# Optimization experiments

Hardware: AMD Instinct MI355X
Metric: run time of the kernel (lower is better)

The kernel has to match this reference:

```python
import jax, jax.numpy as jnp
import numpy as np

NUM_NODES = 100000
NFEAT = 128
EMBED_DIM = 128
NHEADS = 2
NHID = EMBED_DIM // NHEADS  # 64
REL_DIM = 128
NUM_REL = 500
E1 = 288000  # 1-hop edges
E2 = 32000   # 2-hop edges
E = E1 + E2
ALPHA = 0.2  # LeakyReLU slope
EPS = 1e-16


def setup_inputs() -> dict:
    key = jax.random.key(0)
    ks = jax.random.split(key, 10)
    edge_index = jax.random.randint(ks[0], (2, E), 0, NUM_NODES, dtype=jnp.int32)
    x = jax.random.normal(ks[1], (NUM_NODES, NFEAT), dtype=jnp.float32)
    r = jax.random.normal(ks[2], (NUM_REL, REL_DIM), dtype=jnp.float32)
    edge_type = jax.random.randint(ks[3], (E1,), 0, NUM_REL, dtype=jnp.int32)
    edge_type_nhop = jax.random.randint(ks[4], (E2, 2), 0, NUM_REL, dtype=jnp.int32)
    # learned params (get_param -> xavier-ish normal)
    s = 0.02
    W_heads = jax.random.normal(ks[5], (NHEADS, 2 * NFEAT + REL_DIM, NHID), dtype=jnp.float32) * s
    a_heads = jax.random.normal(ks[6], (NHEADS, NHID, 1), dtype=jnp.float32) * s
    W_out = jax.random.normal(ks[7], (2 * (NHID * NHEADS) + EMBED_DIM, NHEADS * NHID), dtype=jnp.float32) * s
    a_out = jax.random.normal(ks[8], (NHEADS * NHID, 1), dtype=jnp.float32) * s
    W_r = jax.random.normal(ks[9], (REL_DIM, EMBED_DIM), dtype=jnp.float32) * s
    return {"edge_index": edge_index, "x": x, "r": r, "edge_type": edge_type,
            "edge_type_nhop": edge_type_nhop, "W_heads": W_heads, "a_heads": a_heads,
            "W_out": W_out, "a_out": a_out, "W_r": W_r}


def _gat_layer(edge_index, x, edge_embed, W, a, concat):
    src = edge_index[0]
    dst = edge_index[1]
    # [E, 2*in + rel] -> [E, out]
    edge_h = jnp.concatenate([x[src], x[dst], edge_embed], axis=1) @ W
    e = jax.nn.leaky_relu(jnp.squeeze(edge_h @ a, axis=-1), negative_slope=ALPHA)  # [E]
    # segment softmax over src groups
    seg_max = jax.ops.segment_max(e, src, num_segments=NUM_NODES)
    w = jnp.exp(e - seg_max[src])
    denom = jax.ops.segment_sum(w, src, num_segments=NUM_NODES)
    att = w / (denom[src] + EPS)  # dropout p=0.0 -> identity
    out = jax.ops.segment_sum(att[:, None] * edge_h, src, num_segments=NUM_NODES)  # [N, out]
    return jax.nn.elu(out) if concat else out


def reference(edge_index, x, r, edge_type, edge_type_nhop, W_heads, a_heads, W_out, a_out, W_r):
    # first-pass relation edge embeddings
    edge_embed = jnp.concatenate(
        [r[edge_type], r[edge_type_nhop[:, 0]] + r[edge_type_nhop[:, 1]]], axis=0)  # [E, rel]
    # multi-head attention layers (concat heads)
    heads = [_gat_layer(edge_index, x, edge_embed, W_heads[h], a_heads[h], True)
             for h in range(NHEADS)]
    x1 = jnp.concatenate(heads, axis=1)  # [N, nheads*nhid]; dropout p=0 identity
    # transform relations
    r2 = r @ W_r  # [num_rel, embed_dim]
    edge_embed2 = jnp.concatenate(
        [r2[edge_type], r2[edge_type_nhop[:, 0]] + r2[edge_type_nhop[:, 1]]], axis=0)
    out = jax.nn.elu(_gat_layer(edge_index, x1, edge_embed2, W_out, a_out, False))
    return out, r2
```

## Files before the change

### kernel.cpp

```cpp
#include <hip/hip_runtime.h>
#include <math.h>

#define NNODES 100000
#define NREL 500
#define E1 288000
#define ETOT 320000
#define LALPHA 0.2f
#define SEPS 1e-16f
#define NB_SCAN ((NNODES + 255) / 256)
#define GTILES 6250
#define GTPB 5
#define GGRID (GTILES / GTPB)

typedef __attribute__((ext_vector_type(8))) short bf16x8;
typedef __attribute__((ext_vector_type(4))) float f32x4;

__device__ __forceinline__ unsigned short f2bf(float x) {
  unsigned int u = __float_as_uint(x);
  unsigned int r = (u + 0x7fffu + ((u >> 16) & 1u)) >> 16;
  return (unsigned short)r;
}
__device__ __forceinline__ unsigned int packbf2(float lo, float hi) {
  return (unsigned int)f2bf(lo) | ((unsigned int)f2bf(hi) << 16);
}
__device__ __forceinline__ float unpk_lo(unsigned int u) { return __uint_as_float(u << 16); }
__device__ __forceinline__ float unpk_hi(unsigned int u) {
  return __uint_as_float(u & 0xffff0000u);
}
__device__ __forceinline__ float lrelu(float e) { return (e >= 0.f) ? e : LALPHA * e; }
__device__ __forceinline__ float wexp(float lg) { return __expf(fminf(lg, 60.f)); }

__device__ __forceinline__ float wave_sum64(float v) {
#pragma unroll
  for (int o = 32; o >= 1; o >>= 1) v += __shfl_xor(v, o, 64);
  return v;
}
__device__ __forceinline__ float red16(float v) {
  v += __shfl_xor(v, 1, 64);
  v += __shfl_xor(v, 2, 64);
  v += __shfl_xor(v, 4, 64);
  v += __shfl_xor(v, 8, 64);
  return v;
}

__global__ void k_zero_int(int* __restrict__ p, int n) {
  int i = blockIdx.x * blockDim.x + threadIdx.x;
  if (i < n) p[i] = 0;
}

__global__ void k_count(const int* __restrict__ src, int* __restrict__ cnt) {
  int e = blockIdx.x * blockDim.x + threadIdx.x;
  if (e < ETOT) atomicAdd(&cnt[src[e]], 1);
}

__global__ void k_scan_a(const int* __restrict__ cnt, int* __restrict__ rowstart,
                         int* __restrict__ blockTot) {
  __shared__ int s[256];
  int t = threadIdx.x;
  int idx = blockIdx.x * 256 + t;
  int v = (idx < NNODES) ? cnt[idx] : 0;
  s[t] = v;
  __syncthreads();
  for (int off = 1; off < 256; off <<= 1) {
    int xv = (t >= off) ? s[t - off] : 0;
    __syncthreads();
    s[t] += xv;
    __syncthreads();
  }
  if (idx < NNODES) rowstart[idx] = s[t] - v;
  if (t == 255) blockTot[blockIdx.x] = s[255];
}

__global__ void k_scan_b(const int* __restrict__ blockTot, int* __restrict__ blockOff) {
  __shared__ int s[512];
  int t = threadIdx.x;
  int v = (t < NB_SCAN) ? blockTot[t] : 0;
  s[t] = v;
  __syncthreads();
  for (int off = 1; off < 512; off <<= 1) {
    int xv = (t >= off) ? s[t - off] : 0;
    __syncthreads();
    s[t] += xv;
    __syncthreads();
  }
  if (t < NB_SCAN) blockOff[t] = s[t] - v;
}

__global__ void k_scan_c(int* __restrict__ rowstart, const int* __restrict__ blockOff,
                         int* __restrict__ cursor) {
  int idx = blockIdx.x * 256 + threadIdx.x;
  if (idx < NNODES) {
    int v = rowstart[idx] + blockOff[blockIdx.x];
    rowstart[idx] = v;
    cursor[idx] = v;
  }
  if (idx == 0) rowstart[NNODES] = ETOT;
}

__global__ void k_scatter(const int* __restrict__ srcA, const int* __restrict__ dstA,
                          const int* __restrict__ et, const int* __restrict__ et2,
                          int* __restrict__ cursor, int* __restrict__ dnp,
                          int2* __restrict__ t12) {
  int e = blockIdx.x * blockDim.x + threadIdx.x;
  if (e < ETOT) {
    int pos = atomicAdd(&cursor[srcA[e]], 1);
    dnp[pos] = dstA[e];
    int t1, t2 = -1;
    if (e < E1) {
      t1 = et[e];
    } else {
      int2 tt = ((const int2*)et2)[e - E1];
      t1 = tt.x;
      t2 = tt.y;
    }
    t12[pos] = make_int2(t1, t2);
  }
}

__global__ void k_relprep1(const float* __restrict__ r, const float* __restrict__ Wh,
                           const float* __restrict__ ah, unsigned int* __restrict__ rW1p,
                           float* __restrict__ srel1) {
  __shared__ float vals[128];
  int t = blockIdx.x;
  int tid = threadIdx.x;
  int h = tid >> 6, kk = tid & 63;
  const float* wcol = Wh + h * 24576 + 256 * 64 + kk;
  const float* rrow = r + t * 128;
  float acc = 0.f;
#pragma unroll 4
  for (int d = 0; d < 128; ++d) acc = fmaf(rrow[d], wcol[d * 64], acc);
  vals[tid] = acc;
  float p = wave_sum64(acc * ah[h * 64 + kk]);
  if (kk == 0) srel1[t * 2 + h] = p;
  __syncthreads();
  if (tid < 64) rW1p[t * 64 + tid] = packbf2(vals[2 * tid], vals[2 * tid + 1]);
}

__global__ void k_relprep2f(const float* __restrict__ r, const float* __restrict__ Wr,
                            const float* __restrict__ Wo, const float* __restrict__ ao,
                            unsigned int* __restrict__ rW2p, float* __restrict__ srel2,
                            float* __restrict__ r2out) {
  __shared__ float v2[128];
  __shared__ float s[128];
  __shared__ float vals[128];
  int t = blockIdx.x;
  int k = threadIdx.x;
  float a2 = 0.f;
#pragma unroll 4
  for (int d = 0; d < 128; ++d) a2 = fmaf(r[t * 128 + d], Wr[d * 128 + k], a2);
  r2out[t * 128 + k] = a2;
  v2[k] = a2;
  __syncthreads();
  float acc = 0.f;
#pragma unroll 4
  for (int d = 0; d < 128; ++d) acc = fmaf(v2[d], Wo[(256 + d) * 128 + k], acc);
  vals[k] = acc;
  s[k] = acc * ao[k];
  __syncthreads();
  for (int off = 64; off >= 1; off >>= 1) {
    if (k < off) s[k] += s[k + off];
    __syncthreads();
  }
  if (k == 0) srel2[t] = s[0];
  if (k < 64) rW2p[t * 64 + k] = packbf2(vals[2 * k], vals[2 * k + 1]);
}

__global__ void k_packb_both(const float* __restrict__ Wh, const float* __restrict__ Wo,
                             unsigned short* __restrict__ Wb1,
                             unsigned short* __restrict__ Wb2) {
  int c = blockIdx.x & 255;
  int layer = blockIdx.x >> 8;
  int d = threadIdx.x;
  if (layer == 0) {
    int h = (c >> 6) & 1, part = c >> 7, kc = c & 63;
    Wb1[c * 128 + d] = f2bf(Wh[h * 24576 + (part * 128 + d) * 64 + kc]);
  } else {
    int part = c >> 7, kc = c & 127;
    Wb2[c * 128 + d] = f2bf(Wo[(part * 128 + d) * 128 + kc]);
  }
}

template <int LAYER>
__global__ __launch_bounds__(256) void k_gemm_mfma(const void* __restrict__ Xin,
                                                   const unsigned short* __restrict__ Wb,
                                                   const float* __restrict__ avec,
                                                   unsigned int* __restrict__ xWp,
                                                   float* __restrict__ sc) {
  const int lane = threadIdx.x & 63;
  const int wave = threadIdx.x >> 6;
  const int colv = lane & 15;
  const int kg = lane >> 4;

  bf16x8 b[4][4];
#pragma unroll
  for (int t = 0; t < 4; ++t)
#pragma unroll
    for (int s = 0; s < 4; ++s)
      b[t][s] = *(const bf16x8*)(Wb + (size_t)(wave * 64 + t * 16 + colv) * 128 + s * 32 +
                                 kg * 8);
  float av[4];
#pragma unroll
  for (int t = 0; t < 4; ++t) av[t] = avec[(wave & 1) * 64 + t * 16 + colv];
  const int slot = (LAYER == 1) ? (((wave & 1) << 1) | (wave >> 1)) : wave;

  const float4* xf4 = (const float4*)Xin;
  const uint4* xu4 = (const uint4*)Xin;
  int tile = blockIdx.x * GTPB;

  float4 cf[8];
  uint4 cu[4];
  {
    int ar = tile * 16 + colv;
    if (LAYER == 1) {
      int base = ar * 32 + kg * 2;
#pragma unroll
      for (int s = 0; s < 4; ++s) {
        cf[2 * s] = xf4[base + s * 8];
        cf[2 * s + 1] = xf4[base + s * 8 + 1];
      }
    } else {
      int base = ar * 16 + kg;
#pragma unroll
      for (int s = 0; s < 4; ++s) cu[s] = xu4[base + s * 4];
    }
  }

  for (int it = 0; it < GTPB; ++it, ++tile) {
    float4 nf[8];
    uint4 nu[4];
    const bool hasnext = (it + 1 < GTPB);
    if (hasnext) {
      int ar = (tile + 1) * 16 + colv;
      if (LAYER == 1) {
        int base = ar * 32 + kg * 2;
#pragma unroll
        for (int s = 0; s < 4; ++s) {
          nf[2 * s] = xf4[base + s * 8];
          nf[2 * s + 1] = xf4[base + s * 8 + 1];
        }
      } else {
        int base = ar * 16 + kg;
#pragma unroll
        for (int s = 0; s < 4; ++s) nu[s] = xu4[base + s * 4];
      }
    }

    bf16x8 a[4];
    if (LAYER == 1) {
#pragma unroll
      for (int s = 0; s < 4; ++s) {
        union {
          unsigned short us[8];
          bf16x8 v;
        } u;
        u.us[0] = f2bf(cf[2 * s].x); u.us[1] = f2bf(cf[2 * s].y);
        u.us[2] = f2bf(cf[2 * s].z); u.us[3] = f2bf(cf[2 * s].w);
        u.us[4] = f2bf(cf[2 * s + 1].x); u.us[5] = f2bf(cf[2 * s + 1].y);
        u.us[6] = f2bf(cf[2 * s + 1].z); u.us[7] = f2bf(cf[2 * s + 1].w);
        a[s] = u.v;
      }
    } else {
#pragma unroll
      for (int s = 0; s < 4; ++s) {
        union {
          uint4 q;
          bf16x8 v;
        } u;
        u.q = cu[s];
        a[s] = u.v;
      }
    }

    f32x4 acc[4];
#pragma unroll
    for (int t = 0; t < 4; ++t) acc[t] = (f32x4){0.f, 0.f, 0.f, 0.f};
#pragma unroll
    for (int s = 0; s < 4; ++s)
#pragma unroll
      for (int t = 0; t < 4; ++t)
        acc[t] = __builtin_amdgcn_mfma_f32_16x16x32_bf16(a[s], b[t][s], acc[t], 0, 0, 0);

    const int rbase = tile * 16 + kg * 4;
    const int m = colv >> 1;
    const bool evn = (colv & 1) == 0;
#pragma unroll
    for (int i = 0; i < 4; ++i) {
      unsigned int* orow = xWp + (size_t)(rbase + i) * 128 + wave * 32;
#pragma unroll
      for (int t = 0; t < 4; ++t) {
        float lo = acc[t][i];
        float other = __shfl_xor(lo, 1, 64);
        if (evn) orow[t * 8 + m] = packbf2(lo, other);
      }
      float p = 0.f;
#pragma unroll
      for (int t = 0; t < 4; ++t) p = fmaf(acc[t][i], av[t], p);
      p = red16(p);
      if (colv == 0) sc[(size_t)(rbase + i) * 4 + slot] = p;
    }

    if (hasnext) {
      if (LAYER == 1) {
#pragma unroll
        for (int j = 0; j < 8; ++j) cf[j] = nf[j];
      } else {
#pragma unroll
        for (int j = 0; j < 4; ++j) cu[j] = nu[j];
      }
    }
  }
}

__global__ __launch_bounds__(256) void k_agg1(
    const int* __restrict__ rowstart, const int* __restrict__ dnp,
    const int2* __restrict__ t12, const unsigned int* __restrict__ xWp,
    const unsigned int* __restrict__ rW1p, const float* __restrict__ sc1,
    const float2* __restrict__ srel1, unsigned int* __restrict__ x1b) {
  int n = blockIdx.x * 4 + (threadIdx.x >> 6);
  int lane = threadIdx.x & 63;
  int q = lane & 15, g = lane >> 4;
  int s0 = rowstart[n];
  int deg = rowstart[n + 1] - s0;
  int jj = q + 16 * g;
  float r0 = 0.f, r1 = 0.f;
  if (deg > 0) {
    float4 scn = ((const float4*)sc1)[n];
    const float ss0 = scn.x, ss1 = scn.z;
    float ac0[4] = {0.f, 0.f, 0.f, 0.f}, ac1[4] = {0.f, 0.f, 0.f, 0.f};
    float dsum0 = 0.f, dsum1 = 0.f;
    const int pend = s0 + deg;
    for (int p0 = s0; p0 < pend; p0 += 4) {
      int p = p0 + g;
      float w0 = 0.f, w1 = 0.f;
      int dne = 0, t1e = 0, t2e = -1;
      if (p < pend) {
        dne = dnp[p];
        int2 tt = t12[p];
        t1e = tt.x;
        t2e = tt.y;
        float2 sr = srel1[t1e];
        float rel0 = sr.x, rel1 = sr.y;
        if (t2e >= 0) {
          float2 sb = srel1[t2e];
          rel0 += sb.x;
          rel1 += sb.y;
        }
        float4 sdv = ((const float4*)sc1)[dne];
        w0 = wexp(lrelu(ss0 + sdv.y + rel0));
        w1 = wexp(lrelu(ss1 + sdv.w + rel1));
        dsum0 += w0;
        dsum1 += w1;
      }
      const unsigned int* xr = xWp + (size_t)dne * 128 + 64;
      const unsigned int* rp = rW1p + (size_t)t1e * 64;
#pragma unroll
      for (int k = 0; k < 4; ++k) {
        int j2 = q + 16 * k;
        float as = (k < 2) ? w0 : w1;
        unsigned int ud = xr[j2];
        unsigned int ur = rp[j2];
        float rv0 = unpk_lo(ur), rv1 = unpk_hi(ur);
        if (t2e >= 0) {
          unsigned int u2 = rW1p[(size_t)t2e * 64 + j2];
          rv0 += unpk_lo(u2);
          rv1 += unpk_hi(u2);
        }
        ac0[k] = fmaf(as, unpk_lo(ud) + rv0, ac0[k]);
        ac1[k] = fmaf(as, unpk_hi(ud) + rv1, ac1[k]);
      }
    }
#pragma unroll
    for (int k = 0; k < 4; ++k) {
      ac0[k] += __shfl_xor(ac0[k], 16, 64);
      ac0[k] += __shfl_xor(ac0[k], 32, 64);
      ac1[k] += __shfl_xor(ac1[k], 16, 64);
      ac1[k] += __shfl_xor(ac1[k], 32, 64);
    }
    dsum0 += __shfl_xor(dsum0, 16, 64);
    dsum0 += __shfl_xor(dsum0, 32, 64);
    dsum1 += __shfl_xor(dsum1, 16, 64);
    dsum1 += __shfl_xor(dsum1, 32, 64);
    float a0g = (g == 0) ? ac0[0] : (g == 1) ? ac0[1] : (g == 2) ? ac0[2] : ac0[3];
    float a1g = (g == 0) ? ac1[0] : (g == 1) ? ac1[1] : (g == 2) ? ac1[2] : ac1[3];
    float dsel = (g < 2) ? dsum0 : dsum1;
    float isel = 1.f / (dsel + SEPS);
    unsigned int us = xWp[(size_t)n * 128 + jj];
    float o0 = (a0g + dsel * unpk_lo(us)) * isel;
    float o1 = (a1g + dsel * unpk_hi(us)) * isel;
    r0 = (o0 > 0.f) ? o0 : __expf(o0) - 1.f;
    r1 = (o1 > 0.f) ? o1 : __expf(o1) - 1.f;
  }
  x1b[(size_t)n * 64 + jj] = packbf2(r0, r1);
}

__global__ __launch_bounds__(256) void k_agg2(
    const int* __restrict__ rowstart, const int* __restrict__ dnp,
    const int2* __restrict__ t12, const unsigned int* __restrict__ xWp,
    const unsigned int* __restrict__ rW2p, const float* __restrict__ sc2,
    const float* __restrict__ srel2, float* __restrict__ outp) {
  int n = blockIdx.x * 4 + (threadIdx.x >> 6);
  int lane = threadIdx.x & 63;
  int q = lane & 15, g = lane >> 4;
  int s0 = rowstart[n];
  int deg = rowstart[n + 1] - s0;
  int jj = q + 16 * g;
  float r0 = 0.f, r1 = 0.f;
  if (deg > 0) {
    float4 scn = ((const float4*)sc2)[n];
    const float ss = scn.x + scn.y;
    float ac0[4] = {0.f, 0.f, 0.f, 0.f}, ac1[4] = {0.f, 0.f, 0.f, 0.f};
    float dsum = 0.f;
    const int pend = s0 + deg;
    for (int p0 = s0; p0 < pend; p0 += 4) {
      int p = p0 + g;
      float w = 0.f;
      int dne = 0, t1e = 0, t2e = -1;
      if (p < pend) {
        dne = dnp[p];
        int2 tt = t12[p];
        t1e = tt.x;
        t2e = tt.y;
        float rel = srel2[t1e];
        if (t2e >= 0) rel += srel2[t2e];
        float4 sdv = ((const float4*)sc2)[dne];
        w = wexp(lrelu(ss + (sdv.z + sdv.w) + rel));
        dsum += w;
      }
      const unsigned int* xr = xWp + (size_t)dne * 128 + 64;
      const unsigned int* rp = rW2p + (size_t)t1e * 64;
#pragma unroll
      for (int k = 0; k < 4; ++k) {
        int j2 = q + 16 * k;
        unsigned int ud = xr[j2];
        unsigned int ur = rp[j2];
        float rv0 = unpk_lo(ur), rv1 = unpk_hi(ur);
        if (t2e >= 0) {
          unsigned int u2 = rW2p[(size_t)t2e * 64 + j2];
          rv0 += unpk_lo(u2);
          rv1 += unpk_hi(u2);
        }
        ac0[k] = fmaf(w, unpk_lo(ud) + rv0, ac0[k]);
        ac1[k] = fmaf(w, unpk_hi(ud) + rv1, ac1[k]);
      }
    }
#pragma unroll
    for (int k = 0; k < 4; ++k) {
      ac0[k] += __shfl_xor(ac0[k], 16, 64);
      ac0[k] += __shfl_xor(ac0[k], 32, 64);
      ac1[k] += __shfl_xor(ac1[k], 16, 64);
      ac1[k] += __shfl_xor(ac1[k], 32, 64);
    }
    dsum += __shfl_xor(dsum, 16, 64);
    dsum += __shfl_xor(dsum, 32, 64);
    float a0g = (g == 0) ? ac0[0] : (g == 1) ? ac0[1] : (g == 2) ? ac0[2] : ac0[3];
    float a1g = (g == 0) ? ac1[0] : (g == 1) ? ac1[1] : (g == 2) ? ac1[2] : ac1[3];
    float inv = 1.f / (dsum + SEPS);
    unsigned int us = xWp[(size_t)n * 128 + jj];
    float o0 = (a0g + dsum * unpk_lo(us)) * inv;
    float o1 = (a1g + dsum * unpk_hi(us)) * inv;
    r0 = (o0 > 0.f) ? o0 : __expf(o0) - 1.f;
    r1 = (o1 > 0.f) ? o1 : __expf(o1) - 1.f;
  }
  ((float2*)outp)[(size_t)n * 64 + jj] = make_float2(r0, r1);
}

extern "C" void kernel_launch(void* const* d_in, const int* in_sizes, int n_in, void* d_out,
                              int out_size, void* d_ws, size_t ws_size, hipStream_t stream) {
  const int* edge_index = (const int*)d_in[0];
  const int* srcA = edge_index;
  const int* dstA = edge_index + ETOT;
  const float* x = (const float*)d_in[1];
  const float* r = (const float*)d_in[2];
  const int* et = (const int*)d_in[3];
  const int* et2 = (const int*)d_in[4];
  const float* Wh = (const float*)d_in[5];
  const float* ah = (const float*)d_in[6];
  const float* Wo = (const float*)d_in[7];
  const float* ao = (const float*)d_in[8];
  const float* Wr = (const float*)d_in[9];
  float* out = (float*)d_out;
  float* r2out = out + (size_t)NNODES * 128;

  char* ws = (char*)d_ws;
  size_t o = 0;
  auto alloc = [&](size_t bytes) {
    char* p = ws + o;
    o += (bytes + 255) & ~(size_t)255;
    return p;
  };
  unsigned int* xWp = (unsigned int*)alloc((size_t)NNODES * 128 * 4);
  float* sc1 = (float*)alloc((size_t)NNODES * 4 * 4);
  float* sc2 = (float*)alloc((size_t)NNODES * 4 * 4);
  unsigned int* rW1p = (unsigned int*)alloc((size_t)NREL * 64 * 4);
  float* srel1 = (float*)alloc(2 * NREL * 4);
  unsigned int* rW2p = (unsigned int*)alloc((size_t)NREL * 64 * 4);
  float* srel2 = (float*)alloc(NREL * 4);
  unsigned int* x1b = (unsigned int*)alloc((size_t)NNODES * 64 * 4);
  unsigned short* Wb1 = (unsigned short*)alloc(256 * 128 * 2);
  unsigned short* Wb2 = (unsigned short*)alloc(256 * 128 * 2);
  int* cnt = (int*)alloc(NNODES * 4);
  int* rowstart = (int*)alloc((NNODES + 1) * 4);
  int* cursor = (int*)alloc(NNODES * 4);
  int* blockTot = (int*)alloc(512 * 4);
  int* blockOff = (int*)alloc(512 * 4);
  int* dnp = (int*)alloc(ETOT * 4);
  int2* t12 = (int2*)alloc((size_t)ETOT * 8);

  const int EB = (ETOT + 255) / 256;

  k_zero_int<<<(NNODES + 255) / 256, 256, 0, stream>>>(cnt, NNODES);
  k_count<<<EB, 256, 0, stream>>>(srcA, cnt);
  k_scan_a<<<NB_SCAN, 256, 0, stream>>>(cnt, rowstart, blockTot);
  k_scan_b<<<1, 512, 0, stream>>>(blockTot, blockOff);
  k_scan_c<<<NB_SCAN, 256, 0, stream>>>(rowstart, blockOff, cursor);
  k_scatter<<<EB, 256, 0, stream>>>(srcA, dstA, et, et2, cursor, dnp, t12);

  k_relprep1<<<NREL, 128, 0, stream>>>(r, Wh, ah, rW1p, srel1);
  k_relprep2f<<<NREL, 128, 0, stream>>>(r, Wr, Wo, ao, rW2p, srel2, r2out);
  k_packb_both<<<512, 128, 0, stream>>>(Wh, Wo, Wb1, Wb2);

  k_gemm_mfma<1><<<GGRID, 256, 0, stream>>>(x, Wb1, ah, xWp, sc1);
  k_agg1<<<NNODES / 4, 256, 0, stream>>>(rowstart, dnp, t12, xWp, rW1p, sc1,
                                         (const float2*)srel1, x1b);

  k_gemm_mfma<2><<<GGRID, 256, 0, stream>>>(x1b, Wb2, ao, xWp, sc2);
  k_agg2<<<NNODES / 4, 256, 0, stream>>>(rowstart, dnp, t12, xWp, rW2p, sc2, srel2, out);
}
```

Measured before the change: 392.7 us.

## Merge prep kernels and fuse scatter with layer-1 GEMM; vectorize aggregation gathers

Folds the edge counting, both relation-projection kernels and the weight packing into one launch, and runs the CSR scatter and the layer-1 MFMA GEMM as separate block ranges of a single kernel. This cuts the number of launches and lets independent work overlap. The aggregation kernels now use 16-byte uint4 gathers per lane with a remapped output column order (jo = 4q+g) instead of four scalar 4-byte loads. That remap has to match the packed GEMM layout, so it carries a risk of permuting columns.

```diff
diff --git a/kernel.cpp b/kernel.cpp
--- a/kernel.cpp
+++ b/kernel.cpp
@@ -11,6 +11,7 @@
 #define GTILES 6250
 #define GTPB 5
 #define GGRID (GTILES / GTPB)
+#define EB 1250
 
 typedef __attribute__((ext_vector_type(8))) short bf16x8;
 typedef __attribute__((ext_vector_type(4))) float f32x4;
@@ -46,11 +47,6 @@
 __global__ void k_zero_int(int* __restrict__ p, int n) {
   int i = blockIdx.x * blockDim.x + threadIdx.x;
   if (i < n) p[i] = 0;
-}
-
-__global__ void k_count(const int* __restrict__ src, int* __restrict__ cnt) {
-  int e = blockIdx.x * blockDim.x + threadIdx.x;
-  if (e < ETOT) atomicAdd(&cnt[src[e]], 1);
 }
 
 __global__ void k_scan_a(const int* __restrict__ cnt, int* __restrict__ rowstart,
@@ -97,95 +93,79 @@
   if (idx == 0) rowstart[NNODES] = ETOT;
 }
 
-__global__ void k_scatter(const int* __restrict__ srcA, const int* __restrict__ dstA,
-                          const int* __restrict__ et, const int* __restrict__ et2,
-                          int* __restrict__ cursor, int* __restrict__ dnp,
-                          int2* __restrict__ t12) {
-  int e = blockIdx.x * blockDim.x + threadIdx.x;
-  if (e < ETOT) {
-    int pos = atomicAdd(&cursor[srcA[e]], 1);
-    dnp[pos] = dstA[e];
-    int t1, t2 = -1;
-    if (e < E1) {
-      t1 = et[e];
+#define PREP_GRID (EB + 250 + 250 + 256)
+__global__ __launch_bounds__(256) void k_prep(
+    const int* __restrict__ srcA, int* __restrict__ cnt, const float* __restrict__ r,
+    const float* __restrict__ Wh, const float* __restrict__ ah,
+    unsigned int* __restrict__ rW1p, float* __restrict__ srel1,
+    const float* __restrict__ Wr, const float* __restrict__ Wo,
+    const float* __restrict__ ao, unsigned int* __restrict__ rW2p,
+    float* __restrict__ srel2, float* __restrict__ r2out,
+    unsigned short* __restrict__ Wb1, unsigned short* __restrict__ Wb2) {
+  __shared__ float sm[6 * 128];
+  const int b = blockIdx.x;
+  const int tid = threadIdx.x;
+  if (b < EB) {
+    int e = b * 256 + tid;
+    if (e < ETOT) atomicAdd(&cnt[srcA[e]], 1);
+  } else if (b < EB + 250) {
+    float(*vals)[128] = (float(*)[128])sm;
+    int rsel = tid >> 7, tid2 = tid & 127;
+    int t = (b - EB) * 2 + rsel;
+    int h = tid2 >> 6, kk = tid2 & 63;
+    const float* wcol = Wh + h * 24576 + 256 * 64 + kk;
+    const float* rrow = r + t * 128;
+    float acc = 0.f;
+#pragma unroll 4
+    for (int d = 0; d < 128; ++d) acc = fmaf(rrow[d], wcol[d * 64], acc);
+    vals[rsel][tid2] = acc;
+    float p = wave_sum64(acc * ah[h * 64 + kk]);
+    if (kk == 0) srel1[t * 2 + h] = p;
+    __syncthreads();
+    if (tid2 < 64) rW1p[t * 64 + tid2] = packbf2(vals[rsel][2 * tid2], vals[rsel][2 * tid2 + 1]);
+  } else if (b < EB + 500) {
+    float(*v2)[128] = (float(*)[128])sm;
+    float(*s)[128] = (float(*)[128])(sm + 2 * 128);
+    float(*vals)[128] = (float(*)[128])(sm + 4 * 128);
+    int rsel = tid >> 7, k = tid & 127;
+    int t = (b - EB - 250) * 2 + rsel;
+    float a2 = 0.f;
+#pragma unroll 4
+    for (int d = 0; d < 128; ++d) a2 = fmaf(r[t * 128 + d], Wr[d * 128 + k], a2);
+    r2out[t * 128 + k] = a2;
+    v2[rsel][k] = a2;
+    __syncthreads();
+    float acc = 0.f;
+#pragma unroll 4
+    for (int d = 0; d < 128; ++d) acc = fmaf(v2[rsel][d], Wo[(256 + d) * 128 + k], acc);
+    vals[rsel][k] = acc;
+    s[rsel][k] = acc * ao[k];
+    __syncthreads();
+    for (int off = 64; off >= 1; off >>= 1) {
+      if (k < off) s[rsel][k] += s[rsel][k + off];
+      __syncthreads();
+    }
+    if (k == 0) srel2[t] = s[rsel][0];
+    if (k < 64) rW2p[t * 64 + k] = packbf2(vals[rsel][2 * k], vals[rsel][2 * k + 1]);
+  } else {
+    int idx = (b - EB - 500) * 2 + (tid >> 7);
+    int layer = idx >> 8, c = idx & 255, d = tid & 127;
+    if (layer == 0) {
+      int h = (c >> 6) & 1, part = c >> 7, kc = c & 63;
+      Wb1[c * 128 + d] = f2bf(Wh[h * 24576 + (part * 128 + d) * 64 + kc]);
     } else {
-      int2 tt = ((const int2*)et2)[e - E1];
-      t1 = tt.x;
-      t2 = tt.y;
-    }
-    t12[pos] = make_int2(t1, t2);
-  }
-}
-
-__global__ void k_relprep1(const float* __restrict__ r, const float* __restrict__ Wh,
-                           const float* __restrict__ ah, unsigned int* __restrict__ rW1p,
-                           float* __restrict__ srel1) {
-  __shared__ float vals[128];
-  int t = blockIdx.x;
-  int tid = threadIdx.x;
-  int h = tid >> 6, kk = tid & 63;
-  const float* wcol = Wh + h * 24576 + 256 * 64 + kk;
-  const float* rrow = r + t * 128;
-  float acc = 0.f;
-#pragma unroll 4
-  for (int d = 0; d < 128; ++d) acc = fmaf(rrow[d], wcol[d * 64], acc);
-  vals[tid] = acc;
-  float p = wave_sum64(acc * ah[h * 64 + kk]);
-  if (kk == 0) srel1[t * 2 + h] = p;
-  __syncthreads();
-  if (tid < 64) rW1p[t * 64 + tid] = packbf2(vals[2 * tid], vals[2 * tid + 1]);
-}
-
-__global__ void k_relprep2f(const float* __restrict__ r, const float* __restrict__ Wr,
-                            const float* __restrict__ Wo, const float* __restrict__ ao,
-                            unsigned int* __restrict__ rW2p, float* __restrict__ srel2,
-                            float* __restrict__ r2out) {
-  __shared__ float v2[128];
-  __shared__ float s[128];
-  __shared__ float vals[128];
-  int t = blockIdx.x;
-  int k = threadIdx.x;
-  float a2 = 0.f;
-#pragma unroll 4
-  for (int d = 0; d < 128; ++d) a2 = fmaf(r[t * 128 + d], Wr[d * 128 + k], a2);
-  r2out[t * 128 + k] = a2;
-  v2[k] = a2;
-  __syncthreads();
-  float acc = 0.f;
-#pragma unroll 4
-  for (int d = 0; d < 128; ++d) acc = fmaf(v2[d], Wo[(256 + d) * 128 + k], acc);
-  vals[k] = acc;
-  s[k] = acc * ao[k];
-  __syncthreads();
-  for (int off = 64; off >= 1; off >>= 1) {
-    if (k < off) s[k] += s[k + off];
-    __syncthreads();
-  }
-  if (k == 0) srel2[t] = s[0];
-  if (k < 64) rW2p[t * 64 + k] = packbf2(vals[2 * k], vals[2 * k + 1]);
-}
-
-__global__ void k_packb_both(const float* __restrict__ Wh, const float* __restrict__ Wo,
-                             unsigned short* __restrict__ Wb1,
-                             unsigned short* __restrict__ Wb2) {
-  int c = blockIdx.x & 255;
-  int layer = blockIdx.x >> 8;
-  int d = threadIdx.x;
-  if (layer == 0) {
-    int h = (c >> 6) & 1, part = c >> 7, kc = c & 63;
-    Wb1[c * 128 + d] = f2bf(Wh[h * 24576 + (part * 128 + d) * 64 + kc]);
-  } else {
-    int part = c >> 7, kc = c & 127;
-    Wb2[c * 128 + d] = f2bf(Wo[(part * 128 + d) * 128 + kc]);
+      int part = c >> 7, kc = c & 127;
+      Wb2[c * 128 + d] = f2bf(Wo[(part * 128 + d) * 128 + kc]);
+    }
   }
 }
 
 template <int LAYER>
-__global__ __launch_bounds__(256) void k_gemm_mfma(const void* __restrict__ Xin,
-                                                   const unsigned short* __restrict__ Wb,
-                                                   const float* __restrict__ avec,
-                                                   unsigned int* __restrict__ xWp,
-                                                   float* __restrict__ sc) {
+__device__ __forceinline__ void gemm_body(int bid, const void* __restrict__ Xin,
+                                          const unsigned short* __restrict__ Wb,
+                                          const float* __restrict__ avec,
+                                          unsigned int* __restrict__ xWp,
+                                          float* __restrict__ sc) {
   const int lane = threadIdx.x & 63;
   const int wave = threadIdx.x >> 6;
   const int colv = lane & 15;
@@ -205,7 +185,7 @@
 
   const float4* xf4 = (const float4*)Xin;
   const uint4* xu4 = (const uint4*)Xin;
-  int tile = blockIdx.x * GTPB;
+  int tile = bid * GTPB;
 
   float4 cf[8];
   uint4 cu[4];
@@ -311,6 +291,40 @@
   }
 }
 
+__global__ __launch_bounds__(256) void k_sg1(
+    const int* __restrict__ srcA, const int* __restrict__ dstA, const int* __restrict__ et,
+    const int* __restrict__ et2, int* __restrict__ cursor, int* __restrict__ dnp,
+    int2* __restrict__ t12, const float* __restrict__ x,
+    const unsigned short* __restrict__ Wb1, const float* __restrict__ ah,
+    unsigned int* __restrict__ xWp, float* __restrict__ sc1) {
+  if (blockIdx.x < EB) {
+    int e = blockIdx.x * 256 + threadIdx.x;
+    if (e < ETOT) {
+      int pos = atomicAdd(&cursor[srcA[e]], 1);
+      dnp[pos] = dstA[e];
+      int t1, t2 = -1;
+      if (e < E1) {
+        t1 = et[e];
+      } else {
+        int2 tt = ((const int2*)et2)[e - E1];
+        t1 = tt.x;
+        t2 = tt.y;
+      }
+      t12[pos] = make_int2(t1, t2);
+    }
+  } else {
+    gemm_body<1>(blockIdx.x - EB, x, Wb1, ah, xWp, sc1);
+  }
+}
+
+__global__ __launch_bounds__(256) void k_gemm2(const void* __restrict__ Xin,
+                                               const unsigned short* __restrict__ Wb,
+                                               const float* __restrict__ avec,
+                                               unsigned int* __restrict__ xWp,
+                                               float* __restrict__ sc) {
+  gemm_body<2>(blockIdx.x, Xin, Wb, avec, xWp, sc);
+}
+
 __global__ __launch_bounds__(256) void k_agg1(
     const int* __restrict__ rowstart, const int* __restrict__ dnp,
     const int2* __restrict__ t12, const unsigned int* __restrict__ xWp,
@@ -321,12 +335,12 @@
   int q = lane & 15, g = lane >> 4;
   int s0 = rowstart[n];
   int deg = rowstart[n + 1] - s0;
-  int jj = q + 16 * g;
+  int jo = 4 * q + g;
   float r0 = 0.f, r1 = 0.f;
   if (deg > 0) {
     float4 scn = ((const float4*)sc1)[n];
     const float ss0 = scn.x, ss1 = scn.z;
-    float ac0[4] = {0.f, 0.f, 0.f, 0.f}, ac1[4] = {0.f, 0.f, 0.f, 0.f};
+    float acL[4] = {0.f, 0.f, 0.f, 0.f}, acH[4] = {0.f, 0.f, 0.f, 0.f};
     float dsum0 = 0.f, dsum1 = 0.f;
     const int pend = s0 + deg;
     for (int p0 = s0; p0 < pend; p0 += 4) {
@@ -351,46 +365,49 @@
         dsum0 += w0;
         dsum1 += w1;
       }
-      const unsigned int* xr = xWp + (size_t)dne * 128 + 64;
-      const unsigned int* rp = rW1p + (size_t)t1e * 64;
-#pragma unroll
-      for (int k = 0; k < 4; ++k) {
-        int j2 = q + 16 * k;
-        float as = (k < 2) ? w0 : w1;
-        unsigned int ud = xr[j2];
-        unsigned int ur = rp[j2];
-        float rv0 = unpk_lo(ur), rv1 = unpk_hi(ur);
-        if (t2e >= 0) {
-          unsigned int u2 = rW1p[(size_t)t2e * 64 + j2];
-          rv0 += unpk_lo(u2);
-          rv1 += unpk_hi(u2);
-        }
-        ac0[k] = fmaf(as, unpk_lo(ud) + rv0, ac0[k]);
-        ac1[k] = fmaf(as, unpk_hi(ud) + rv1, ac1[k]);
-      }
+      uint4 xd = *(const uint4*)(xWp + (size_t)dne * 128 + 64 + 4 * q);
+      uint4 rv = *(const uint4*)(rW1p + (size_t)t1e * 64 + 4 * q);
+      float rL[4] = {unpk_lo(rv.x), unpk_lo(rv.y), unpk_lo(rv.z), unpk_lo(rv.w)};
+      float rH[4] = {unpk_hi(rv.x), unpk_hi(rv.y), unpk_hi(rv.z), unpk_hi(rv.w)};
+      if (t2e >= 0) {
+        uint4 r2v = *(const uint4*)(rW1p + (size_t)t2e * 64 + 4 * q);
+        rL[0] += unpk_lo(r2v.x); rH[0] += unpk_hi(r2v.x);
+        rL[1] += unpk_lo(r2v.y); rH[1] += unpk_hi(r2v.y);
+        rL[2] += unpk_lo(r2v.z); rH[2] += unpk_hi(r2v.z);
+        rL[3] += unpk_lo(r2v.w); rH[3] += unpk_hi(r2v.w);
+      }
+      float wq = (q < 8) ? w0 : w1;
+      acL[0] = fmaf(wq, unpk_lo(xd.x) + rL[0], acL[0]);
+      acH[0] = fmaf(wq, unpk_hi(xd.x) + rH[0], acH[0]);
+      acL[1] = fmaf(wq, unpk_lo(xd.y) + rL[1], acL[1]);
+      acH[1] = fmaf(wq, unpk_hi(xd.y) + rH[1], acH[1]);
+      acL[2] = fmaf(wq, unpk_lo(xd.z) + rL[2], acL[2]);
+      acH[2] = fmaf(wq, unpk_hi(xd.z) + rH[2], acH[2]);
+      acL[3] = fmaf(wq, unpk_lo(xd.w) + rL[3], acL[3]);
+      acH[3] = fmaf(wq, unpk_hi(xd.w) + rH[3], acH[3]);
     }
 #pragma unroll
     for (int k = 0; k < 4; ++k) {
-      ac0[k] += __shfl_xor(ac0[k], 16, 64);
-      ac0[k] += __shfl_xor(ac0[k], 32, 64);
-      ac1[k] += __shfl_xor(ac1[k], 16, 64);
-      ac1[k] += __shfl_xor(ac1[k], 32, 64);
+      acL[k] += __shfl_xor(acL[k], 16, 64);
+      acL[k] += __shfl_xor(acL[k], 32, 64);
+      acH[k] += __shfl_xor(acH[k], 16, 64);
+      acH[k] += __shfl_xor(acH[k], 32, 64);
     }
     dsum0 += __shfl_xor(dsum0, 16, 64);
     dsum0 += __shfl_xor(dsum0, 32, 64);
     dsum1 += __shfl_xor(dsum1, 16, 64);
     dsum1 += __shfl_xor(dsum1, 32, 64);
-    float a0g = (g == 0) ? ac0[0] : (g == 1) ? ac0[1] : (g == 2) ? ac0[2] : ac0[3];
-    float a1g = (g == 0) ? ac1[0] : (g == 1) ? ac1[1] : (g == 2) ? ac1[2] : ac1[3];
-    float dsel = (g < 2) ? dsum0 : dsum1;
+    float aL = (g == 0) ? acL[0] : (g == 1) ? acL[1] : (g == 2) ? acL[2] : acL[3];
+    float aH = (g == 0) ? acH[0] : (g == 1) ? acH[1] : (g == 2) ? acH[2] : acH[3];
+    float dsel = (q < 8) ? dsum0 : dsum1;
     float isel = 1.f / (dsel + SEPS);
-    unsigned int us = xWp[(size_t)n * 128 + jj];
-    float o0 = (a0g + dsel * unpk_lo(us)) * isel;
-    float o1 = (a1g + dsel * unpk_hi(us)) * isel;
+    unsigned int us = xWp[(size_t)n * 128 + jo];
+    float o0 = (aL + dsel * unpk_lo(us)) * isel;
+    float o1 = (aH + dsel * unpk_hi(us)) * isel;
     r0 = (o0 > 0.f) ? o0 : __expf(o0) - 1.f;
     r1 = (o1 > 0.f) ? o1 : __expf(o1) - 1.f;
   }
-  x1b[(size_t)n * 64 + jj] = packbf2(r0, r1);
+  x1b[(size_t)n * 64 + jo] = packbf2(r0, r1);
 }
 
 __global__ __launch_bounds__(256) void k_agg2(
@@ -403,12 +420,12 @@
   int q = lane & 15, g = lane >> 4;
   int s0 = rowstart[n];
   int deg = rowstart[n + 1] - s0;
-  int jj = q + 16 * g;
+  int jo = 4 * q + g;
   float r0 = 0.f, r1 = 0.f;
   if (deg > 0) {
     float4 scn = ((const float4*)sc2)[n];
     const float ss = scn.x + scn.y;
-    float ac0[4] = {0.f, 0.f, 0.f, 0.f}, ac1[4] = {0.f, 0.f, 0.f, 0.f};
+    float acL[4] = {0.f, 0.f, 0.f, 0.f}, acH[4] = {0.f, 0.f, 0.f, 0.f};
     float dsum = 0.f;
     const int pend = s0 + deg;
     for (int p0 = s0; p0 < pend; p0 += 4) {
@@ -426,42 +443,45 @@
         w = wexp(lrelu(ss + (sdv.z + sdv.w) + rel));
         dsum += w;
       }
-      const unsigned int* xr = xWp + (size_t)dne * 128 + 64;
-      const unsigned int* rp = rW2p + (size_t)t1e * 64;
-#pragma unroll
-      for (int k = 0; k < 4; ++k) {
-        int j2 = q + 16 * k;
-        unsigned int ud = xr[j2];
-        unsigned int ur = rp[j2];
-        float rv0 = unpk_lo(ur), rv1 = unpk_hi(ur);
-        if (t2e >= 0) {
-          unsigned int u2 = rW2p[(size_t)t2e * 64 + j2];
-          rv0 += unpk_lo(u2);
-          rv1 += unpk_hi(u2);
-        }
-        ac0[k] = fmaf(w, unpk_lo(ud) + rv0, ac0[k]);
-        ac1[k] = fmaf(w, unpk_hi(ud) + rv1, ac1[k]);
-      }
+      uint4 xd = *(const uint4*)(xWp + (size_t)dne * 128 + 64 + 4 * q);
+      uint4 rv = *(const uint4*)(rW2p + (size_t)t1e * 64 + 4 * q);
+      float rL[4] = {unpk_lo(rv.x), unpk_lo(rv.y), unpk_lo(rv.z), unpk_lo(rv.w)};
+      float rH[4] = {unpk_hi(rv.x), unpk_hi(rv.y), unpk_hi(rv.z), unpk_hi(rv.w)};
+      if (t2e >= 0) {
+        uint4 r2v = *(const uint4*)(rW2p + (size_t)t2e * 64 + 4 * q);
+        rL[0] += unpk_lo(r2v.x); rH[0] += unpk_hi(r2v.x);
+        rL[1] += unpk_lo(r2v.y); rH[1] += unpk_hi(r2v.y);
+        rL[2] += unpk_lo(r2v.z); rH[2] += unpk_hi(r2v.z);
+        rL[3] += unpk_lo(r2v.w); rH[3] += unpk_hi(r2v.w);
+      }
+      acL[0] = fmaf(w, unpk_lo(xd.x) + rL[0], acL[0]);
+      acH[0] = fmaf(w, unpk_hi(xd.x) + rH[0], acH[0]);
+      acL[1] = fmaf(w, unpk_lo(xd.y) + rL[1], acL[1]);
+      acH[1] = fmaf(w, unpk_hi(xd.y) + rH[1], acH[1]);
+      acL[2] = fmaf(w, unpk_lo(xd.z) + rL[2], acL[2]);
+      acH[2] = fmaf(w, unpk_hi(xd.z) + rH[2], acH[2]);
+      acL[3] = fmaf(w, unpk_lo(xd.w) + rL[3], acL[3]);
+      acH[3] = fmaf(w, unpk_hi(xd.w) + rH[3], acH[3]);
     }
 #pragma unroll
     for (int k = 0; k < 4; ++k) {
-      ac0[k] += __shfl_xor(ac0[k], 16, 64);
-      ac0[k] += __shfl_xor(ac0[k], 32, 64);
-      ac1[k] += __shfl_xor(ac1[k], 16, 64);
-      ac1[k] += __shfl_xor(ac1[k], 32, 64);
+      acL[k] += __shfl_xor(acL[k], 16, 64);
+      acL[k] += __shfl_xor(acL[k], 32, 64);
+      acH[k] += __shfl_xor(acH[k], 16, 64);
+      acH[k] += __shfl_xor(acH[k], 32, 64);
     }
     dsum += __shfl_xor(dsum, 16, 64);
     dsum += __shfl_xor(dsum, 32, 64);
-    float a0g = (g == 0) ? ac0[0] : (g == 1) ? ac0[1] : (g == 2) ? ac0[2] : ac0[3];
-    float a1g = (g == 0) ? ac1[0] : (g == 1) ? ac1[1] : (g == 2) ? ac1[2] : ac1[3];
+    float aL = (g == 0) ? acL[0] : (g == 1) ? acL[1] : (g == 2) ? acL[2] : acL[3];
+    float aH = (g == 0) ? acH[0] : (g == 1) ? acH[1] : (g == 2) ? acH[2] : acH[3];
     float inv = 1.f / (dsum + SEPS);
-    unsigned int us = xWp[(size_t)n * 128 + jj];
-    float o0 = (a0g + dsum * unpk_lo(us)) * inv;
-    float o1 = (a1g + dsum * unpk_hi(us)) * inv;
+    unsigned int us = xWp[(size_t)n * 128 + jo];
+    float o0 = (aL + dsum * unpk_lo(us)) * inv;
+    float o1 = (aH + dsum * unpk_hi(us)) * inv;
     r0 = (o0 > 0.f) ? o0 : __expf(o0) - 1.f;
     r1 = (o1 > 0.f) ? o1 : __expf(o1) - 1.f;
   }
-  ((float2*)outp)[(size_t)n * 64 + jj] = make_float2(r0, r1);
+  ((float2*)outp)[(size_t)n * 64 + jo] = make_float2(r0, r1);
 }
 
 extern "C" void kernel_launch(void* const* d_in, const int* in_sizes, int n_in, void* d_out,
@@ -506,23 +526,16 @@
   int* dnp = (int*)alloc(ETOT * 4);
   int2* t12 = (int2*)alloc((size_t)ETOT * 8);
 
-  const int EB = (ETOT + 255) / 256;
-
   k_zero_int<<<(NNODES + 255) / 256, 256, 0, stream>>>(cnt, NNODES);
-  k_count<<<EB, 256, 0, stream>>>(srcA, cnt);
+  k_prep<<<PREP_GRID, 256, 0, stream>>>(srcA, cnt, r, Wh, ah, rW1p, srel1, Wr, Wo, ao, rW2p,
+                                        srel2, r2out, Wb1, Wb2);
   k_scan_a<<<NB_SCAN, 256, 0, stream>>>(cnt, rowstart, blockTot);
   k_scan_b<<<1, 512, 0, stream>>>(blockTot, blockOff);
   k_scan_c<<<NB_SCAN, 256, 0, stream>>>(rowstart, blockOff, cursor);
-  k_scatter<<<EB, 256, 0, stream>>>(srcA, dstA, et, et2, cursor, dnp, t12);
-
-  k_relprep1<<<NREL, 128, 0, stream>>>(r, Wh, ah, rW1p, srel1);
-  k_relprep2f<<<NREL, 128, 0, stream>>>(r, Wr, Wo, ao, rW2p, srel2, r2out);
-  k_packb_both<<<512, 128, 0, stream>>>(Wh, Wo, Wb1, Wb2);
-
-  k_gemm_mfma<1><<<GGRID, 256, 0, stream>>>(x, Wb1, ah, xWp, sc1);
+  k_sg1<<<EB + GGRID, 256, 0, stream>>>(srcA, dstA, et, et2, cursor, dnp, t12, x, Wb1, ah,
+                                        xWp, sc1);
   k_agg1<<<NNODES / 4, 256, 0, stream>>>(rowstart, dnp, t12, xWp, rW1p, sc1,
                                          (const float2*)srel1, x1b);
-
-  k_gemm_mfma<2><<<GGRID, 256, 0, stream>>>(x1b, Wb2, ao, xWp, sc2);
+  k_gemm2<<<GGRID, 256, 0, stream>>>(x1b, Wb2, ao, xWp, sc2);
   k_agg2<<<NNODES / 4, 256, 0, stream>>>(rowstart, dnp, t12, xWp, rW2p, sc2, srel2, out);
 }
```

Result: faster. 348.7 us (-11.2%).
